# Performance work log

Hardware: AMD Instinct MI355X
Metric: run time of the kernel (lower is better)

Reference implementation:

```python
import jax, jax.numpy as jnp
import numpy as np

N_HEAD = 16
D_HEAD = 64
D_MODEL = 1024
N_ROLL = 3
SCALE = 1.0 / (D_HEAD ** 0.5)
EPS = 1e-5


def mul_roll_repeat(x, n_roll):
    # concat of x * roll(x, i) over i=1..n_roll along last dim
    return jnp.concatenate([x * jnp.roll(x, i, axis=-1) for i in range(1, n_roll + 1)], axis=-1)


def dpfp(x):
    # DPFP feature map: [relu(x), relu(-x)] then roll-multiply-repeat
    x2 = jnp.concatenate([jax.nn.relu(x), jax.nn.relu(-x)], axis=-1)
    return mul_roll_repeat(x2, N_ROLL)


def layer_norm(x, gamma, beta):
    mu = jnp.mean(x, axis=-1, keepdims=True)
    var = jnp.var(x, axis=-1, keepdims=True)
    return (x - mu) * jax.lax.rsqrt(var + 1e-5) * gamma + beta


def setup_inputs() -> dict:
    key = jax.random.key(0)
    ks = jax.random.split(key, 4)
    S, B = 2048, 2
    h = jax.random.normal(ks[0], (S, B, D_MODEL), dtype=jnp.float32)
    Wq = jax.random.normal(ks[1], (D_MODEL, N_HEAD * D_HEAD), dtype=jnp.float32) * 0.02
    Wkv = jax.random.normal(ks[2], (D_MODEL, 2 * N_HEAD * D_HEAD), dtype=jnp.float32) * 0.02
    Wo = jax.random.normal(ks[3], (N_HEAD * D_HEAD, D_MODEL), dtype=jnp.float32) * 0.02
    ln_gamma = jnp.ones((D_MODEL,), dtype=jnp.float32)
    ln_beta = jnp.zeros((D_MODEL,), dtype=jnp.float32)
    return {"h": h, "Wq": Wq, "Wkv": Wkv, "Wo": Wo, "ln_gamma": ln_gamma, "ln_beta": ln_beta}


def reference(h, Wq, Wkv, Wo, ln_gamma, ln_beta):
    # h: [S, B, D_MODEL]; mems=None, attn_mask=None, post-LN, eval (no dropout)
    S, B, _ = h.shape
    q = (h @ Wq).reshape(S, B, N_HEAD, D_HEAD)
    kv = h @ Wkv
    k, v = jnp.split(kv, 2, axis=-1)
    k = k.reshape(S, B, N_HEAD, D_HEAD)
    v = v.reshape(S, B, N_HEAD, D_HEAD)

    pq = dpfp(q)  # [S, B, N, F], F = 2*D_HEAD*N_ROLL = 384
    pk = dpfp(k)

    # Linear-attention form: identical math to the original quadratic
    # einsum('ibnd,jbnd->ijbn') * scale, summed over j for the denominator,
    # since there is no mask and dropatt=0. Avoids the O(S^2) score tensor.
    kv_agg = jnp.einsum('jbnf,jbnd->bnfd', pk, v)          # [B, N, F, D]
    z = pk.sum(axis=0)                                      # [B, N, F]
    num = jnp.einsum('ibnf,bnfd->ibnd', pq, kv_agg) * SCALE  # [S, B, N, D]
    den = jnp.einsum('ibnf,bnf->ibn', pq, z) * SCALE + EPS   # [S, B, N]
    attn_vec = (num / den[..., None]).reshape(S, B, N_HEAD * D_HEAD)

    attn_out = attn_vec @ Wo
    return layer_norm(h + attn_out, ln_gamma, ln_beta)
```

## Files before the change

### kernel.cpp

```cpp
#include <hip/hip_runtime.h>
#include <math.h>

#define NH 16
#define DM 1024
#define FEAT 384
#define SB 4096
#define SEQ 2048

static constexpr float SCALE = 0.125f;
static constexpr float EPS = 1e-5f;

typedef __attribute__((ext_vector_type(8))) _Float16 half8;
typedef __attribute__((ext_vector_type(4))) _Float16 half4;
typedef __attribute__((ext_vector_type(4))) float f32x4;

#define AS1 __attribute__((address_space(1)))
#define AS3 __attribute__((address_space(3)))

#define IDX(r, o) ((((r) << 6)) + ((((o) ^ ((r) & 7))) << 3))

__global__ __launch_bounds__(256) void prep_kernel(const float* __restrict__ h,
                                                   const float* __restrict__ Wq,
                                                   const float* __restrict__ Wkv,
                                                   const float* __restrict__ Wo,
                                                   _Float16* __restrict__ h_h,
                                                   _Float16* __restrict__ WqkvT,
                                                   _Float16* __restrict__ WoT) {
    __shared__ _Float16 tile[32][33];
    int bid = blockIdx.x, t = threadIdx.x;
    if (bid < 4096) {
        int i = bid * 256 + t;
        const float4 v = ((const float4*)h)[i];
        half4 o = {(_Float16)v.x, (_Float16)v.y, (_Float16)v.z, (_Float16)v.w};
        ((half4*)h_h)[i] = o;
        return;
    }
    const float* src;
    _Float16* dst;
    int N, col0, n0, k0;
    if (bid < 7168) {
        int b2 = bid - 4096;
        n0 = (b2 % 96) * 32; k0 = (b2 / 96) * 32;
        if (n0 < 1024) { src = Wq; N = 1024; col0 = n0; }
        else           { src = Wkv; N = 2048; col0 = n0 - 1024; }
        dst = WqkvT;
    } else {
        int b3 = bid - 7168;
        n0 = (b3 & 31) * 32; k0 = (b3 >> 5) * 32;
        src = Wo; N = 1024; col0 = n0; dst = WoT;
    }
    int tx = t & 31, ty = t >> 5;
    #pragma unroll
    for (int i = 0; i < 4; ++i)
        tile[ty + i * 8][tx] = (_Float16)src[(size_t)(k0 + ty + i * 8) * N + col0 + tx];
    __syncthreads();
    #pragma unroll
    for (int i = 0; i < 4; ++i)
        dst[(size_t)(n0 + ty + i * 8) * 1024 + k0 + tx] = tile[tx][ty + i * 8];
}

template <int MH>
__device__ __forceinline__ void mfma_all(f32x4 (&acc)[8][3], half8 (&a)[4][2],
                                         half8 (&bv)[3][2]) {
    #pragma unroll
    for (int mf = 0; mf < 4; ++mf)
        #pragma unroll
        for (int nf = 0; nf < 3; ++nf)
            #pragma unroll
            for (int ks = 0; ks < 2; ++ks)
                acc[MH * 4 + mf][nf] = __builtin_amdgcn_mfma_f32_16x16x32_f16(
                    a[mf][ks], bv[nf][ks], acc[MH * 4 + mf][nf], 0, 0, 0);
}

__global__ __launch_bounds__(512) void gemm_f16_8ph(const _Float16* __restrict__ A,
                                                    const _Float16* __restrict__ BT,
                                                    _Float16* __restrict__ C,
                                                    int M, int N, int K) {
    __shared__ _Float16 smem[57344];
    const int t = threadIdx.x;
    const int w = t >> 6, l = t & 63;
    const int wr = w >> 2, wc = w & 3;
    const int NT = K >> 6;
    const int NU = K >> 4;

    int nwg = gridDim.x;
    int cpx = nwg >> 3;
    int bid = blockIdx.x;
    int swz = (bid & 7) * cpx + (bid >> 3);
    int ntile = N / 192;
    int row0 = (swz / ntile) << 8;
    int col0 = (swz % ntile) * 192;

    f32x4 acc[8][3];
    #pragma unroll
    for (int m = 0; m < 8; ++m)
        #pragma unroll
        for (int n = 0; n < 3; ++n)
            acc[m][n] = (f32x4){0.f, 0.f, 0.f, 0.f};

    const int lr = l >> 3;
    const int lc8 = ((l & 7) ^ lr) * 8;

    auto STAGE = [&](int s) {
        if (s >= NU) return;
        int tau = s >> 2, u = s & 3;
        int kk = tau << 6;
        int bufo = (tau & 1) * 28672;
        if (u == 0) {
            #pragma unroll
            for (int i = 0; i < 2; ++i) {
                int chunk = w * 2 + i;
                const _Float16* src = BT + (size_t)(col0 + chunk * 8 + lr) * K + kk + lc8;
                __builtin_amdgcn_global_load_lds((const AS1 void*)src,
                    (AS3 void*)(smem + bufo + 16384 + chunk * 512), 16, 0, 0);
            }
        } else if (u == 1) {
            const _Float16* src = BT + (size_t)(col0 + 128 + w * 8 + lr) * K + kk + lc8;
            __builtin_amdgcn_global_load_lds((const AS1 void*)src,
                (AS3 void*)(smem + bufo + 24576 + w * 512), 16, 0, 0);
        } else {
            int rbase = (u == 3) ? 128 : 0;
            int lbase = (u == 3) ? 8192 : 0;
            #pragma unroll
            for (int i = 0; i < 2; ++i) {
                int chunk = w * 2 + i;
                const _Float16* src = A + (size_t)(row0 + rbase + chunk * 8 + lr) * K + kk + lc8;
                __builtin_amdgcn_global_load_lds((const AS1 void*)src,
                    (AS3 void*)(smem + bufo + lbase + chunk * 512), 16, 0, 0);
            }
        }
    };

    half8 a[4][2], bv[3][2];
    auto LDA = [&](int mh, int bufo) {
        #pragma unroll
        for (int mf = 0; mf < 4; ++mf) {
            int r = wr * 128 + (mh * 4 + mf) * 16 + (l & 15);
            #pragma unroll
            for (int ks = 0; ks < 2; ++ks) {
                int c16 = (ks * 4 + (l >> 4)) ^ (r & 7);
                a[mf][ks] = *(const half8*)&smem[bufo + r * 64 + c16 * 8];
            }
        }
    };
    auto LDB = [&](int bufo) {
        #pragma unroll
        for (int nf = 0; nf < 3; ++nf) {
            int r = wc * 48 + nf * 16 + (l & 15);
            #pragma unroll
            for (int ks = 0; ks < 2; ++ks) {
                int c16 = (ks * 4 + (l >> 4)) ^ (r & 7);
                bv[nf][ks] = *(const half8*)&smem[bufo + 16384 + r * 64 + c16 * 8];
            }
        }
    };

    STAGE(0); STAGE(1);
    STAGE(2); STAGE(3);
    STAGE(4); STAGE(5);
    asm volatile("s_waitcnt vmcnt(3)" ::: "memory");
    __builtin_amdgcn_s_barrier();

    #pragma unroll 1
    for (int ti = 0; ti < NT; ++ti) {
        const int bufo = (ti & 1) * 28672;
        const int sb = (ti + 1) << 2;
        LDA(0, bufo); LDB(bufo);
        STAGE(sb + 2); STAGE(sb + 3);
        __builtin_amdgcn_sched_barrier(0);
        __builtin_amdgcn_s_barrier();
        asm volatile("s_waitcnt lgkmcnt(0)" ::: "memory");
        __builtin_amdgcn_sched_barrier(0);
        __builtin_amdgcn_s_setprio(1);
        mfma_all<0>(acc, a, bv);
        __builtin_amdgcn_s_setprio(0);
        __builtin_amdgcn_sched_barrier(0);
        __builtin_amdgcn_s_barrier();
        LDA(1, bufo);
        STAGE(sb + 4); STAGE(sb + 5);
        __builtin_amdgcn_sched_barrier(0);
        __builtin_amdgcn_s_barrier();
        asm volatile("s_waitcnt lgkmcnt(0)" ::: "memory");
        __builtin_amdgcn_sched_barrier(0);
        __builtin_amdgcn_s_setprio(1);
        mfma_all<1>(acc, a, bv);
        __builtin_amdgcn_s_setprio(0);
        __builtin_amdgcn_sched_barrier(0);
        if (ti < NT - 2) asm volatile("s_waitcnt vmcnt(3)" ::: "memory");
        else             asm volatile("s_waitcnt vmcnt(0)" ::: "memory");
        __builtin_amdgcn_s_barrier();
    }

    int ocol = l & 15, orow4 = (l >> 4) * 4;
    #pragma unroll
    for (int mf = 0; mf < 8; ++mf)
        #pragma unroll
        for (int nf = 0; nf < 3; ++nf) {
            size_t base = (size_t)(row0 + wr * 128 + mf * 16 + orow4) * N
                        + col0 + wc * 48 + nf * 16 + ocol;
            #pragma unroll
            for (int j = 0; j < 4; ++j)
                C[base + (size_t)j * N] = (_Float16)acc[mf][nf][j];
        }
}

__global__ __launch_bounds__(256) void gemm_f16(const _Float16* __restrict__ A,
                                                const _Float16* __restrict__ BT,
                                                _Float16* __restrict__ C,
                                                int M, int N, int K) {
    __shared__ _Float16 Asb[128 * 32];
    __shared__ _Float16 Bsb[128 * 32];
    int t = threadIdx.x;
    int w = t >> 6, l = t & 63;
    int wr = w >> 1, wc = w & 1;
    int row0 = blockIdx.y * 128, col0 = blockIdx.x * 128;

    f32x4 acc[4][4];
    #pragma unroll
    for (int m = 0; m < 4; ++m)
        #pragma unroll
        for (int n = 0; n < 4; ++n)
            acc[m][n] = (f32x4){0.f, 0.f, 0.f, 0.f};

    int srow = l >> 2;
    int scol = (l & 3) * 8;

    for (int k0 = 0; k0 < K; k0 += 32) {
        #pragma unroll
        for (int i = 0; i < 2; ++i) {
            int chunk = w * 2 + i;
            const _Float16* asrc =
                A + (size_t)(row0 + chunk * 16 + srow) * K + k0 + scol;
            __builtin_amdgcn_global_load_lds((const AS1 void*)asrc,
                                             (AS3 void*)(Asb + chunk * 512), 16, 0, 0);
            const _Float16* bsrc =
                BT + (size_t)(col0 + chunk * 16 + srow) * K + k0 + scol;
            __builtin_amdgcn_global_load_lds((const AS1 void*)bsrc,
                                             (AS3 void*)(Bsb + chunk * 512), 16, 0, 0);
        }
        __syncthreads();
        int rsel = l & 15, csel = (l >> 4) * 8;
        half8 a[4], b[4];
        #pragma unroll
        for (int m = 0; m < 4; ++m)
            a[m] = *(const half8*)&Asb[(wr * 64 + m * 16 + rsel) * 32 + csel];
        #pragma unroll
        for (int n = 0; n < 4; ++n)
            b[n] = *(const half8*)&Bsb[(wc * 64 + n * 16 + rsel) * 32 + csel];
        #pragma unroll
        for (int m = 0; m < 4; ++m)
            #pragma unroll
            for (int n = 0; n < 4; ++n)
                acc[m][n] = __builtin_amdgcn_mfma_f32_16x16x32_f16(a[m], b[n], acc[m][n], 0, 0, 0);
        __syncthreads();
    }

    int ocol = l & 15, orow = (l >> 4) * 4;
    #pragma unroll
    for (int m = 0; m < 4; ++m)
        #pragma unroll
        for (int n = 0; n < 4; ++n) {
            size_t base = (size_t)(row0 + wr * 64 + m * 16 + orow) * N
                        + col0 + wc * 64 + n * 16 + ocol;
            #pragma unroll
            for (int j = 0; j < 4; ++j)
                C[base + (size_t)j * N] = (_Float16)acc[m][n][j];
        }
}

__global__ __launch_bounds__(512) void kvagg_fused(const _Float16* __restrict__ qkv,
                                                   float* __restrict__ kvp,
                                                   float* __restrict__ zp) {
    __shared__ _Float16 x2s[128 * 64];
    __shared__ _Float16 vTs[64 * 64];
    __shared__ _Float16 pkTs[384 * 64];
    const int t = threadIdx.x;
    const int w = t >> 6, l = t & 63;
    const int bn = blockIdx.x;
    const int jseg = blockIdx.y;
    const int b = bn >> 4, nh = bn & 15;

    f32x4 acc[4][3];
    #pragma unroll
    for (int mf = 0; mf < 4; ++mf)
        #pragma unroll
        for (int nf = 0; nf < 3; ++nf)
            acc[mf][nf] = (f32x4){0.f, 0.f, 0.f, 0.f};
    float zacc[3] = {0.f, 0.f, 0.f};

    const int sc = t & 63;
    const int so = t >> 6;

    #pragma unroll 1
    for (int ch = 0; ch < 4; ++ch) {
        int j0 = jseg * 256 + ch * 64;
        _Float16 kx[8], vx[8];
        #pragma unroll
        for (int e = 0; e < 8; ++e) {
            size_t rb = (size_t)((j0 + so * 8 + e) * 2 + b) * 3072 + nh * 64 + sc;
            kx[e] = qkv[rb + 1024];
            vx[e] = qkv[rb + 2048];
        }
        half8 xlo, xhi, vv;
        #pragma unroll
        for (int e = 0; e < 8; ++e) {
            float kf = (float)kx[e];
            xlo[e] = (_Float16)fmaxf(kf, 0.f);
            xhi[e] = (_Float16)fmaxf(-kf, 0.f);
            vv[e] = vx[e];
        }
        if (ch) __syncthreads();
        *(half8*)&x2s[IDX(sc, so)] = xlo;
        *(half8*)&x2s[IDX(sc + 64, so)] = xhi;
        *(half8*)&vTs[IDX(sc, so)] = vv;
        __syncthreads();
        {
            const int o = t & 7;
            const int fb = t >> 3;
            #pragma unroll
            for (int it = 0; it < 6; ++it) {
                int f = it * 64 + fb;
                int fm = f & 127;
                int r = (f >> 7) + 1;
                int fm2 = (fm - r) & 127;
                half8 pa = *(const half8*)&x2s[IDX(fm, o)];
                half8 pb = *(const half8*)&x2s[IDX(fm2, o)];
                *(half8*)&pkTs[IDX(f, o)] = pa * pb;
            }
        }
        __syncthreads();
        #pragma unroll
        for (int ks = 0; ks < 2; ++ks) {
            half8 a[4], bq[3];
            int oo = ks * 4 + (l >> 4);
            #pragma unroll
            for (int mf = 0; mf < 4; ++mf) {
                int dr = mf * 16 + (l & 15);
                a[mf] = *(const half8*)&vTs[IDX(dr, oo)];
            }
            #pragma unroll
            for (int nf = 0; nf < 3; ++nf) {
                int fr = w * 48 + nf * 16 + (l & 15);
                bq[nf] = *(const half8*)&pkTs[IDX(fr, oo)];
                #pragma unroll
                for (int e = 0; e < 8; ++e) zacc[nf] += (float)bq[nf][e];
            }
            #pragma unroll
            for (int mf = 0; mf < 4; ++mf)
                #pragma unroll
                for (int nf = 0; nf < 3; ++nf)
                    acc[mf][nf] = __builtin_amdgcn_mfma_f32_16x16x32_f16(
                        a[mf], bq[nf], acc[mf][nf], 0, 0, 0);
        }
    }

    #pragma unroll
    for (int nf = 0; nf < 3; ++nf) {
        float v = zacc[nf];
        v += __shfl_xor(v, 16, 64);
        v += __shfl_xor(v, 32, 64);
        if (l < 16)
            zp[(size_t)(jseg * 32 + bn) * FEAT + w * 48 + nf * 16 + l] = v;
    }
    float* outp = kvp + (size_t)(jseg * 32 + bn) * 64 * FEAT;
    int orow = (l >> 4) * 4, ocol = l & 15;
    #pragma unroll
    for (int mf = 0; mf < 4; ++mf)
        #pragma unroll
        for (int nf = 0; nf < 3; ++nf) {
            int fcol = w * 48 + nf * 16 + ocol;
            #pragma unroll
            for (int j = 0; j < 4; ++j)
                outp[(size_t)(mf * 16 + orow + j) * FEAT + fcol] = acc[mf][nf][j];
        }
}

__global__ __launch_bounds__(256) void reduceA(const float* __restrict__ kvp,
                                               const float* __restrict__ zp,
                                               _Float16* __restrict__ kvaggT,
                                               float* __restrict__ z) {
    const int NKV = 32 * 64 * FEAT;
    int idx = blockIdx.x * 256 + threadIdx.x;
    if (idx < NKV) {
        float s = 0.f;
        #pragma unroll
        for (int c = 0; c < 8; ++c) s += kvp[(size_t)c * NKV + idx];
        kvaggT[idx] = (_Float16)s;
    } else if (idx < NKV + 32 * FEAT) {
        int e = idx - NKV;
        float s = 0.f;
        #pragma unroll
        for (int c = 0; c < 8; ++c) s += zp[c * 32 * FEAT + e];
        z[e] = s;
    }
}

#define X2STR 152
__global__ __launch_bounds__(256) void attn_fused(const _Float16* __restrict__ qkv,
                                                  const _Float16* __restrict__ kvaggT,
                                                  const float* __restrict__ z,
                                                  _Float16* __restrict__ av) {
    __shared__ _Float16 x2e[64 * X2STR];
    __shared__ _Float16 B_lds[64 * FEAT];
    __shared__ float z_lds[FEAT];
    __shared__ float den_lds[64];
    const int t = threadIdx.x;
    const int w = t >> 6, l = t & 63;
    const int iblk = blockIdx.x;
    const int bn = blockIdx.y;
    const int b = bn >> 4, nh = bn & 15;

    {
        const _Float16* Bg = kvaggT + (size_t)bn * 64 * FEAT;
        #pragma unroll
        for (int s = 0; s < 12; ++s) {
            int idx8 = t + 256 * s;
            int row = idx8 / 48, c16 = idx8 - row * 48;
            half8 vv = *(const half8*)&Bg[row * FEAT + c16 * 8];
            *(half8*)&B_lds[row * FEAT + ((c16 ^ (row & 7)) << 3)] = vv;
        }
    }
    for (int e = t; e < FEAT; e += 256) z_lds[e] = z[(size_t)bn * FEAT + e];

    {
        int row = t >> 2, c0 = (t & 3) * 16;
        const _Float16* qrow = qkv + (size_t)((iblk * 64 + row) * 2 + b) * 3072 + nh * 64;
        half8 q0 = *(const half8*)&qrow[c0];
        half8 q1 = *(const half8*)&qrow[c0 + 8];
        half8 lo0, lo1, hi0, hi1;
        #pragma unroll
        for (int e = 0; e < 8; ++e) {
            float f0 = (float)q0[e], f1 = (float)q1[e];
            lo0[e] = (_Float16)fmaxf(f0, 0.f);
            lo1[e] = (_Float16)fmaxf(f1, 0.f);
            hi0[e] = (_Float16)fmaxf(-f0, 0.f);
            hi1[e] = (_Float16)fmaxf(-f1, 0.f);
        }
        _Float16* xr = &x2e[row * X2STR];
        *(half8*)&xr[c0] = lo0;
        *(half8*)&xr[c0 + 8] = lo1;
        *(half8*)&xr[64 + c0] = hi0;
        *(half8*)&xr[64 + c0 + 8] = hi1;
        if (c0 == 0) { *(half8*)&xr[128] = lo0; *(half8*)&xr[136] = lo1; }
        if (c0 == 16) { *(half8*)&xr[144] = lo0; }
    }
    __syncthreads();

    const int rloc16 = l & 15;
    const int csel = (l >> 4) * 8;
    const int lrow = w * 16 + rloc16;
    half8 y8[16];
    {
        const _Float16* xr = &x2e[lrow * X2STR + csel];
        #pragma unroll
        for (int j = 0; j < 16; ++j)
            y8[j] = *(const half8*)&xr[j * 8];
    }
    half8 afr[12];
    #pragma unroll
    for (int ks = 0; ks < 12; ++ks) {
        const int r = (ks >> 2) + 1;
        #pragma unroll
        for (int e = 0; e < 8; ++e) {
            const int j1 = ((ks & 3) * 32 + e) & 127;
            const int j2 = ((ks & 3) * 32 + e - r) & 127;
            afr[ks][e] = y8[j1 >> 3][j1 & 7] * y8[j2 >> 3][j2 & 7];
        }
    }

    f32x4 acc[4];
    #pragma unroll
    for (int n = 0; n < 4; ++n) acc[n] = (f32x4){0.f, 0.f, 0.f, 0.f};
    float den = 0.f;
    #pragma unroll
    for (int ks = 0; ks < 12; ++ks) {
        #pragma unroll
        for (int e = 0; e < 8; ++e)
            den += (float)afr[ks][e] * z_lds[ks * 32 + csel + e];
        #pragma unroll
        for (int nf = 0; nf < 4; ++nf) {
            int row = nf * 16 + rloc16;
            int c16 = (ks * 4 + (l >> 4)) ^ (row & 7);
            half8 bfr = *(const half8*)&B_lds[row * FEAT + (c16 << 3)];
            acc[nf] = __builtin_amdgcn_mfma_f32_16x16x32_f16(afr[ks], bfr, acc[nf], 0, 0, 0);
        }
    }

    den += __shfl_xor(den, 16, 64);
    den += __shfl_xor(den, 32, 64);
    if (l < 16) den_lds[w * 16 + l] = den;
    __syncthreads();

    #pragma unroll
    for (int nf = 0; nf < 4; ++nf)
        #pragma unroll
        for (int j = 0; j < 4; ++j) {
            int rl = w * 16 + (l >> 4) * 4 + j;
            float dv = den_lds[rl] * SCALE + EPS;
            float val = acc[nf][j] * SCALE / dv;
            int i = iblk * 64 + rl;
            av[((size_t)i * 2 + b) * 1024 + nh * 64 + nf * 16 + (l & 15)] = (_Float16)val;
        }
}

__global__ __launch_bounds__(256) void ln_kernel(const float* __restrict__ h,
                                                 const _Float16* __restrict__ attn_out,
                                                 const float* __restrict__ gamma,
                                                 const float* __restrict__ beta,
                                                 float* __restrict__ out) {
    int r = blockIdx.x;
    int t = threadIdx.x;
    const float4 hv = ((const float4*)(h + (size_t)r * 1024))[t];
    const half4 a4 = ((const half4*)(attn_out + (size_t)r * 1024))[t];
    float x[4] = {hv.x + (float)a4[0], hv.y + (float)a4[1],
                  hv.z + (float)a4[2], hv.w + (float)a4[3]};
    float sum = x[0] + x[1] + x[2] + x[3];
    float sq = x[0]*x[0] + x[1]*x[1] + x[2]*x[2] + x[3]*x[3];
    #pragma unroll
    for (int off = 32; off >= 1; off >>= 1) {
        sum += __shfl_xor(sum, off, 64);
        sq += __shfl_xor(sq, off, 64);
    }
    __shared__ float ssum[4], ssq[4];
    int wl = t >> 6, lane = t & 63;
    if (lane == 0) { ssum[wl] = sum; ssq[wl] = sq; }
    __syncthreads();
    sum = ssum[0] + ssum[1] + ssum[2] + ssum[3];
    sq = ssq[0] + ssq[1] + ssq[2] + ssq[3];
    float mu = sum * (1.f / 1024.f);
    float var = sq * (1.f / 1024.f) - mu * mu;
    float rs = rsqrtf(var + 1e-5f);
    const float4 g4 = ((const float4*)gamma)[t];
    const float4 b4 = ((const float4*)beta)[t];
    float4 o;
    o.x = (x[0] - mu) * rs * g4.x + b4.x;
    o.y = (x[1] - mu) * rs * g4.y + b4.y;
    o.z = (x[2] - mu) * rs * g4.z + b4.z;
    o.w = (x[3] - mu) * rs * g4.w + b4.w;
    ((float4*)(out + (size_t)r * 1024))[t] = o;
}

extern "C" void kernel_launch(void* const* d_in, const int* in_sizes, int n_in,
                              void* d_out, int out_size, void* d_ws, size_t ws_size,
                              hipStream_t stream) {
    const float* h     = (const float*)d_in[0];
    const float* Wq    = (const float*)d_in[1];
    const float* Wkv   = (const float*)d_in[2];
    const float* Wo    = (const float*)d_in[3];
    const float* gamma = (const float*)d_in[4];
    const float* beta  = (const float*)d_in[5];
    float* out = (float*)d_out;
    _Float16* u = (_Float16*)d_ws;

    _Float16* h_h    = u;
    _Float16* WqkvT  = u + 4194304;
    _Float16* WoT    = u + 7340032;
    _Float16* qkv    = u + 8388608;
    float*    kvp    = (float*)(u + 20971520);
    float*    zp     = (float*)(u + 33554432);
    _Float16* kvaggT = u + 33751040;
    float*    z      = (float*)(u + 34537472);
    _Float16* av         = h_h;
    _Float16* attn_out_h = qkv;

    dim3 blk(256);
    prep_kernel<<<dim3(8192), blk, 0, stream>>>(h, Wq, Wkv, Wo, h_h, WqkvT, WoT);
    gemm_f16_8ph<<<dim3(256), dim3(512), 0, stream>>>(h_h, WqkvT, qkv, SB, 3072, DM);
    kvagg_fused<<<dim3(32, 8), dim3(512), 0, stream>>>(qkv, kvp, zp);
    reduceA<<<dim3(3120), blk, 0, stream>>>(kvp, zp, kvaggT, z);
    attn_fused<<<dim3(32, 32), blk, 0, stream>>>(qkv, kvaggT, z, av);
    gemm_f16<<<dim3(8, 32), blk, 0, stream>>>(av, WoT, attn_out_h, SB, 1024, DM);
    ln_kernel<<<dim3(SB), blk, 0, stream>>>(h, attn_out_h, gamma, beta, out);
}
```

Baseline: 108.4 us.

## Triple-buffer Wo GEMM with swizzled LDS and store partial KV sums in fp16

New measurement: 99.33 us. 1.09x faster.

```diff
diff --git a/kernel.cpp b/kernel.cpp
--- a/kernel.cpp
+++ b/kernel.cpp
@@ -204,15 +204,15 @@
         }
 }
 
-__global__ __launch_bounds__(256) void gemm_f16(const _Float16* __restrict__ A,
-                                                const _Float16* __restrict__ BT,
-                                                _Float16* __restrict__ C,
-                                                int M, int N, int K) {
-    __shared__ _Float16 Asb[128 * 32];
-    __shared__ _Float16 Bsb[128 * 32];
-    int t = threadIdx.x;
-    int w = t >> 6, l = t & 63;
-    int wr = w >> 1, wc = w & 1;
+__global__ __launch_bounds__(256) void gemm_wo(const _Float16* __restrict__ A,
+                                               const _Float16* __restrict__ BT,
+                                               _Float16* __restrict__ C,
+                                               int M, int N, int K) {
+    __shared__ _Float16 smem[3 * 16384];
+    const int t = threadIdx.x;
+    const int w = t >> 6, l = t & 63;
+    const int wr = w >> 1, wc = w & 1;
+    const int NT = K >> 6;
     int row0 = blockIdx.y * 128, col0 = blockIdx.x * 128;
 
     f32x4 acc[4][4];
@@ -222,54 +222,86 @@
         for (int n = 0; n < 4; ++n)
             acc[m][n] = (f32x4){0.f, 0.f, 0.f, 0.f};
 
-    int srow = l >> 2;
-    int scol = (l & 3) * 8;
-
-    for (int k0 = 0; k0 < K; k0 += 32) {
-        #pragma unroll
-        for (int i = 0; i < 2; ++i) {
-            int chunk = w * 2 + i;
-            const _Float16* asrc =
-                A + (size_t)(row0 + chunk * 16 + srow) * K + k0 + scol;
+    const int lr = l >> 3;
+    const int lc8 = ((l & 7) ^ lr) * 8;
+
+    auto STAGE = [&](int ti) {
+        if (ti >= NT) return;
+        int kk = ti << 6;
+        int bufo = (ti % 3) * 16384;
+        #pragma unroll
+        for (int i = 0; i < 4; ++i) {
+            int chunk = w * 4 + i;
+            const _Float16* asrc = A + (size_t)(row0 + chunk * 8 + lr) * K + kk + lc8;
             __builtin_amdgcn_global_load_lds((const AS1 void*)asrc,
-                                             (AS3 void*)(Asb + chunk * 512), 16, 0, 0);
-            const _Float16* bsrc =
-                BT + (size_t)(col0 + chunk * 16 + srow) * K + k0 + scol;
+                (AS3 void*)(smem + bufo + chunk * 512), 16, 0, 0);
+            const _Float16* bsrc = BT + (size_t)(col0 + chunk * 8 + lr) * K + kk + lc8;
             __builtin_amdgcn_global_load_lds((const AS1 void*)bsrc,
-                                             (AS3 void*)(Bsb + chunk * 512), 16, 0, 0);
-        }
-        __syncthreads();
-        int rsel = l & 15, csel = (l >> 4) * 8;
-        half8 a[4], b[4];
-        #pragma unroll
-        for (int m = 0; m < 4; ++m)
-            a[m] = *(const half8*)&Asb[(wr * 64 + m * 16 + rsel) * 32 + csel];
-        #pragma unroll
-        for (int n = 0; n < 4; ++n)
-            b[n] = *(const half8*)&Bsb[(wc * 64 + n * 16 + rsel) * 32 + csel];
-        #pragma unroll
-        for (int m = 0; m < 4; ++m)
-            #pragma unroll
-            for (int n = 0; n < 4; ++n)
-                acc[m][n] = __builtin_amdgcn_mfma_f32_16x16x32_f16(a[m], b[n], acc[m][n], 0, 0, 0);
-        __syncthreads();
+                (AS3 void*)(smem + bufo + 8192 + chunk * 512), 16, 0, 0);
+        }
+    };
+
+    STAGE(0); STAGE(1);
+    asm volatile("s_waitcnt vmcnt(8)" ::: "memory");
+    __builtin_amdgcn_s_barrier();
+
+    #pragma unroll 1
+    for (int ti = 0; ti < NT; ++ti) {
+        const int bufo = (ti % 3) * 16384;
+        half8 a[4][2], bv[4][2];
+        #pragma unroll
+        for (int mf = 0; mf < 4; ++mf) {
+            int r = wr * 64 + mf * 16 + (l & 15);
+            #pragma unroll
+            for (int ks = 0; ks < 2; ++ks) {
+                int c16 = (ks * 4 + (l >> 4)) ^ (r & 7);
+                a[mf][ks] = *(const half8*)&smem[bufo + r * 64 + c16 * 8];
+            }
+        }
+        #pragma unroll
+        for (int nf = 0; nf < 4; ++nf) {
+            int r = wc * 64 + nf * 16 + (l & 15);
+            #pragma unroll
+            for (int ks = 0; ks < 2; ++ks) {
+                int c16 = (ks * 4 + (l >> 4)) ^ (r & 7);
+                bv[nf][ks] = *(const half8*)&smem[bufo + 8192 + r * 64 + c16 * 8];
+            }
+        }
+        STAGE(ti + 2);
+        __builtin_amdgcn_sched_barrier(0);
+        asm volatile("s_waitcnt lgkmcnt(0)" ::: "memory");
+        __builtin_amdgcn_sched_barrier(0);
+        __builtin_amdgcn_s_setprio(1);
+        #pragma unroll
+        for (int mf = 0; mf < 4; ++mf)
+            #pragma unroll
+            for (int nf = 0; nf < 4; ++nf)
+                #pragma unroll
+                for (int ks = 0; ks < 2; ++ks)
+                    acc[mf][nf] = __builtin_amdgcn_mfma_f32_16x16x32_f16(
+                        a[mf][ks], bv[nf][ks], acc[mf][nf], 0, 0, 0);
+        __builtin_amdgcn_s_setprio(0);
+        __builtin_amdgcn_sched_barrier(0);
+        if (ti < NT - 2) asm volatile("s_waitcnt vmcnt(8)" ::: "memory");
+        else             asm volatile("s_waitcnt vmcnt(0)" ::: "memory");
+        __builtin_amdgcn_s_barrier();
     }
 
     int ocol = l & 15, orow = (l >> 4) * 4;
     #pragma unroll
-    for (int m = 0; m < 4; ++m)
-        #pragma unroll
-        for (int n = 0; n < 4; ++n) {
-            size_t base = (size_t)(row0 + wr * 64 + m * 16 + orow) * N
-                        + col0 + wc * 64 + n * 16 + ocol;
+    for (int mf = 0; mf < 4; ++mf)
+        #pragma unroll
+        for (int nf = 0; nf < 4; ++nf) {
+            size_t base = (size_t)(row0 + wr * 64 + mf * 16 + orow) * N
+                        + col0 + wc * 64 + nf * 16 + ocol;
             #pragma unroll
             for (int j = 0; j < 4; ++j)
-                C[base + (size_t)j * N] = (_Float16)acc[m][n][j];
+                C[base + (size_t)j * N] = (_Float16)acc[mf][nf][j];
         }
 }
 
 __global__ __launch_bounds__(512) void kvagg_fused(const _Float16* __restrict__ qkv,
-                                                   float* __restrict__ kvp,
+                                                   _Float16* __restrict__ kvp,
                                                    float* __restrict__ zp) {
     __shared__ _Float16 x2s[128 * 64];
     __shared__ _Float16 vTs[64 * 64];
@@ -362,7 +394,7 @@
         if (l < 16)
             zp[(size_t)(jseg * 32 + bn) * FEAT + w * 48 + nf * 16 + l] = v;
     }
-    float* outp = kvp + (size_t)(jseg * 32 + bn) * 64 * FEAT;
+    _Float16* outp = kvp + (size_t)(jseg * 32 + bn) * 64 * FEAT;
     int orow = (l >> 4) * 4, ocol = l & 15;
     #pragma unroll
     for (int mf = 0; mf < 4; ++mf)
@@ -371,11 +403,11 @@
             int fcol = w * 48 + nf * 16 + ocol;
             #pragma unroll
             for (int j = 0; j < 4; ++j)
-                outp[(size_t)(mf * 16 + orow + j) * FEAT + fcol] = acc[mf][nf][j];
-        }
-}
-
-__global__ __launch_bounds__(256) void reduceA(const float* __restrict__ kvp,
+                outp[(size_t)(mf * 16 + orow + j) * FEAT + fcol] = (_Float16)acc[mf][nf][j];
+        }
+}
+
+__global__ __launch_bounds__(256) void reduceA(const _Float16* __restrict__ kvp,
                                                const float* __restrict__ zp,
                                                _Float16* __restrict__ kvaggT,
                                                float* __restrict__ z) {
@@ -384,7 +416,7 @@
     if (idx < NKV) {
         float s = 0.f;
         #pragma unroll
-        for (int c = 0; c < 8; ++c) s += kvp[(size_t)c * NKV + idx];
+        for (int c = 0; c < 8; ++c) s += (float)kvp[(size_t)c * NKV + idx];
         kvaggT[idx] = (_Float16)s;
     } else if (idx < NKV + 32 * FEAT) {
         int e = idx - NKV;
@@ -556,7 +588,7 @@
     _Float16* WqkvT  = u + 4194304;
     _Float16* WoT    = u + 7340032;
     _Float16* qkv    = u + 8388608;
-    float*    kvp    = (float*)(u + 20971520);
+    _Float16* kvp    = u + 20971520;
     float*    zp     = (float*)(u + 33554432);
     _Float16* kvaggT = u + 33751040;
     float*    z      = (float*)(u + 34537472);
@@ -569,6 +601,6 @@
     kvagg_fused<<<dim3(32, 8), dim3(512), 0, stream>>>(qkv, kvp, zp);
     reduceA<<<dim3(3120), blk, 0, stream>>>(kvp, zp, kvaggT, z);
     attn_fused<<<dim3(32, 32), blk, 0, stream>>>(qkv, kvaggT, z, av);
-    gemm_f16<<<dim3(8, 32), blk, 0, stream>>>(av, WoT, attn_out_h, SB, 1024, DM);
+    gemm_wo<<<dim3(8, 32), blk, 0, stream>>>(av, WoT, attn_out_h, SB, 1024, DM);
     ln_kernel<<<dim3(SB), blk, 0, stream>>>(h, attn_out_h, gamma, beta, out);
 }
```
